# Kernel tuning notes

Hardware: AMD Instinct MI355X
Metric: run time of the kernel (lower is better)

The kernel has to match this reference:

```python
import jax, jax.numpy as jnp
import numpy as np

N_NODES = 100000
N_EDGES = 500000
D = 128          # node embedding dim; in_channels = 2*D = 256
HID = 256
OUT = 1


def setup_inputs() -> dict:
    key = jax.random.key(0)
    k1, k2, k3, k4, k5 = jax.random.split(key, 5)
    z = jax.random.normal(k1, (N_NODES, D), dtype=jnp.float32)
    z2 = jax.random.normal(k2, (N_NODES, D), dtype=jnp.float32)
    edge = jax.random.randint(k3, (2, N_EDGES), 0, N_NODES, dtype=jnp.int64)
    # MLP params (Linear stored as [in, out] for x @ W + b)
    W1 = jax.random.normal(k4, (2 * D, HID), dtype=jnp.float32) * (1.0 / np.sqrt(2 * D))
    b1 = jnp.zeros((HID,), dtype=jnp.float32)
    W2 = jax.random.normal(k5, (HID, OUT), dtype=jnp.float32) * (1.0 / np.sqrt(HID))
    b2 = jnp.zeros((OUT,), dtype=jnp.float32)
    return {"z": z, "z2": z2, "edge": edge, "W1": W1, "b1": b1, "W2": W2, "b2": b2}


def reference(z, z2, edge, W1, b1, W2, b2):
    # Gather node embeddings at edge endpoints, elementwise multiply, concat.
    src, dst = edge[0], edge[1]
    x = jnp.concatenate([z[src] * z[dst], z2[src] * z2[dst]], axis=1)  # [E, 2D]
    # Two-layer MLP (dropout is identity in eval mode), relu, final sigmoid.
    h = jax.nn.relu(x @ W1 + b1)        # [E, HID]
    out = jax.nn.sigmoid(h @ W2 + b2)   # [E, 1]
    return out
```

## Files before the change

kernel.cpp:

```cpp
#include <hip/hip_runtime.h>
#include <hip/hip_bf16.h>
#include <math.h>

typedef _Float16 half4 __attribute__((ext_vector_type(4)));
typedef _Float16 half8 __attribute__((ext_vector_type(8)));
typedef float f32x4 __attribute__((ext_vector_type(4)));

#define NE 500000
#define ND 128
#define NNODES 100000
#define NT ((NE + 63) / 64)
#define ZI_BLOCKS 12500

__global__ __launch_bounds__(256) void prep_all_kernel(
    const float* __restrict__ z, const float* __restrict__ z2,
    _Float16* __restrict__ zi,
    const float* __restrict__ W1, _Float16* __restrict__ w1p) {
    if (blockIdx.x < ZI_BLOCKS) {
        long t = (long)blockIdx.x * 256 + threadIdx.x;
        long idx = t * 8;
        int node = (int)(idx >> 8), col = (int)(idx & 255);
        const float* src = (col < 128) ? (z + (long)node * 128 + col)
                                       : (z2 + (long)node * 128 + (col - 128));
        float4 a = *reinterpret_cast<const float4*>(src);
        float4 b = *reinterpret_cast<const float4*>(src + 4);
        half8 v;
        v[0] = (_Float16)a.x; v[1] = (_Float16)a.y;
        v[2] = (_Float16)a.z; v[3] = (_Float16)a.w;
        v[4] = (_Float16)b.x; v[5] = (_Float16)b.y;
        v[6] = (_Float16)b.z; v[7] = (_Float16)b.w;
        *reinterpret_cast<half8*>(zi + idx) = v;
    } else {
        int i = (blockIdx.x - ZI_BLOCKS) * 256 + threadIdx.x;
        int j = i & 7;
        int lane = (i >> 3) & 63;
        int ks = (i >> 9) & 7;
        int nf = (i >> 12) & 3;
        int ni = i >> 14;
        int col = ni * 64 + nf * 16 + (lane & 15);
        int k = ks * 32 + (lane >> 4) * 8 + j;
        w1p[i] = (_Float16)W1[(long)k * 256 + col];
    }
}

template<int MIRROR>
__global__ __launch_bounds__(256, 4) void edge_mlp_v11(
    const float* __restrict__ z, const float* __restrict__ z2,
    const _Float16* __restrict__ zi,
    const int* __restrict__ edge,
    const _Float16* __restrict__ w1p,
    const float* __restrict__ b1, const float* __restrict__ W2,
    const float* __restrict__ b2, float* __restrict__ out)
{
    __shared__ _Float16 xs[64 * 256];
    __shared__ float ps[256];

    const int tid = threadIdx.x;
    const int lane = tid & 63;
    const int wv = tid >> 6;
    const int l15 = lane & 15;
    const int l4 = lane >> 4;
    const long eb0 = (long)blockIdx.x * 64;

    int idx;
    {
        long e = eb0 + wv * 16 + l15; if (e >= NE) e = NE - 1;
        idx = edge[(((lane >> 4) & 1) ? (long)NE : 0L) + e];
    }

    float b1v[4], w2v[4];
#pragma unroll
    for (int nf = 0; nf < 4; ++nf) {
        int col = wv * 64 + nf * 16 + l15;
        b1v[nf] = b1[col];
        w2v[nf] = W2[col];
    }
    const float bias2 = b2[0];

    if (MIRROR) {
        half4 vs[8], vd[8];
#pragma unroll
        for (int b = 0; b < 2; ++b) {
#pragma unroll
            for (int j = 0; j < 8; ++j) {
                int s = __builtin_amdgcn_readlane(idx, b * 8 + j);
                int d = __builtin_amdgcn_readlane(idx, 16 + b * 8 + j);
                vs[j] = *reinterpret_cast<const half4*>(zi + (long)s * 256 + lane * 4);
                vd[j] = *reinterpret_cast<const half4*>(zi + (long)d * 256 + lane * 4);
            }
#pragma unroll
            for (int j = 0; j < 8; ++j) {
                int e = wv * 16 + b * 8 + j;
                half4 p = vs[j] * vd[j];
                *reinterpret_cast<half4*>(
                    (char*)xs + e * 512 + ((lane * 8) ^ ((e & 7) << 4))) = p;
            }
        }
    } else {
        const float* zs = (lane < 32) ? z : z2;
        const int coff = (lane & 31) * 4;
#pragma unroll
        for (int b = 0; b < 4; ++b) {
            float4 fs[4], fd[4];
#pragma unroll
            for (int j = 0; j < 4; ++j) {
                int s = __builtin_amdgcn_readlane(idx, b * 4 + j);
                int d = __builtin_amdgcn_readlane(idx, 16 + b * 4 + j);
                fs[j] = *reinterpret_cast<const float4*>(zs + (long)s * ND + coff);
                fd[j] = *reinterpret_cast<const float4*>(zs + (long)d * ND + coff);
            }
#pragma unroll
            for (int j = 0; j < 4; ++j) {
                int e = wv * 16 + b * 4 + j;
                half4 p;
                p[0] = (_Float16)(fs[j].x * fd[j].x);
                p[1] = (_Float16)(fs[j].y * fd[j].y);
                p[2] = (_Float16)(fs[j].z * fd[j].z);
                p[3] = (_Float16)(fs[j].w * fd[j].w);
                *reinterpret_cast<half4*>(
                    (char*)xs + e * 512 + ((lane * 8) ^ ((e & 7) << 4))) = p;
            }
        }
    }
    __syncthreads();

    f32x4 acc[4][4];
#pragma unroll
    for (int mf = 0; mf < 4; ++mf)
#pragma unroll
        for (int nf = 0; nf < 4; ++nf)
            acc[mf][nf] = (f32x4){b1v[nf], b1v[nf], b1v[nf], b1v[nf]};

#pragma unroll
    for (int ks = 0; ks < 8; ++ks) {
        const int kb = ks * 64 + l4 * 16;
        half8 a[4], bfr[4];
#pragma unroll
        for (int mf = 0; mf < 4; ++mf) {
            int r = mf * 16 + l15;
            a[mf] = *reinterpret_cast<const half8*>(
                (const char*)xs + r * 512 + (kb ^ ((r & 7) << 4)));
        }
#pragma unroll
        for (int nf = 0; nf < 4; ++nf)
            bfr[nf] = *reinterpret_cast<const half8*>(
                w1p + (wv * 32 + nf * 8 + ks) * 512 + lane * 8);
#pragma unroll
        for (int mf = 0; mf < 4; ++mf)
#pragma unroll
            for (int nf = 0; nf < 4; ++nf)
                acc[mf][nf] = __builtin_amdgcn_mfma_f32_16x16x32_f16(
                    a[mf], bfr[nf], acc[mf][nf], 0, 0, 0);
    }

    float v[16];
#pragma unroll
    for (int mf = 0; mf < 4; ++mf)
#pragma unroll
        for (int r = 0; r < 4; ++r) {
            float s = 0.f;
#pragma unroll
            for (int nf = 0; nf < 4; ++nf)
                s += fmaxf(acc[mf][nf][r], 0.f) * w2v[nf];
            v[mf * 4 + r] = s;
        }
#pragma unroll
    for (int j = 0; j < 4; ++j) {
        const int m = 1 << j;
        const bool hi = (l15 & m) != 0;
#pragma unroll
        for (int p = 0; p < 16; p += 2 * m) {
            float snd = hi ? v[p] : v[p + m];
            float rcv = __shfl_xor(snd, m, 64);
            float kept = hi ? v[p + m] : v[p];
            v[p] = kept + rcv;
        }
    }
    {
        int row = (l15 >> 2) * 16 + l4 * 4 + (l15 & 3);
        ps[wv * 64 + row] = v[0];
    }
    __syncthreads();

    if (tid < 64) {
        float p = ps[tid] + ps[64 + tid] + ps[128 + tid] + ps[192 + tid] + bias2;
        long e = eb0 + tid;
        if (e < NE) out[e] = 1.0f / (1.0f + expf(-p));
    }
}

extern "C" void kernel_launch(void* const* d_in, const int* in_sizes, int n_in,
                              void* d_out, int out_size, void* d_ws, size_t ws_size,
                              hipStream_t stream)
{
    const float* z  = (const float*)d_in[0];
    const float* z2 = (const float*)d_in[1];
    const int*  edge = (const int*)d_in[2];
    const float* W1 = (const float*)d_in[3];
    const float* b1 = (const float*)d_in[4];
    const float* W2 = (const float*)d_in[5];
    const float* b2 = (const float*)d_in[6];
    float* out = (float*)d_out;

    const size_t zi_bytes = (size_t)NNODES * 256 * 2;
    const size_t w1_bytes = 256 * 256 * 2;
    const bool mirrors = (ws_size >= zi_bytes + w1_bytes);

    _Float16* zi  = (_Float16*)d_ws;
    _Float16* w1p = mirrors ? (_Float16*)((char*)d_ws + zi_bytes)
                            : (_Float16*)d_ws;

    if (mirrors) {
        prep_all_kernel<<<ZI_BLOCKS + 256, 256, 0, stream>>>(z, z2, zi, W1, w1p);
        edge_mlp_v11<1><<<NT, 256, 0, stream>>>(
            z, z2, zi, edge, w1p, b1, W2, b2, out);
    } else {
        prep_all_kernel<<<256, 256, 0, stream>>>(z, z2, (_Float16*)nullptr, W1, w1p);
        edge_mlp_v11<0><<<NT, 256, 0, stream>>>(
            z, z2, (const _Float16*)nullptr, edge, w1p, b1, W2, b2, out);
    }
}
```

Baseline: 132.3 us.

## Bucket-sort edges by source node before the fused edge MLP

Adds a histogram, a single-block scan and an atomic scatter pass that reorder edges into buckets keyed on source node index divided by 8. The main MLP kernel then reads the reordered source/destination indices and writes each result back to its original edge position. The aim is better cache locality for the source-side embedding gathers. In exchange it adds three extra kernel launches, atomic contention, extra index traffic and scattered output writes, while destination gathers stay random.

```diff
diff --git a/kernel.cpp b/kernel.cpp
--- a/kernel.cpp
+++ b/kernel.cpp
@@ -11,11 +11,20 @@
 #define NNODES 100000
 #define NT ((NE + 63) / 64)
 #define ZI_BLOCKS 12500
+#define W1_BLOCKS 256
+#define HIST_BLOCKS 977
+#define NB 12504
+
+__global__ __launch_bounds__(256) void zero_hist_kernel(int* __restrict__ hist) {
+    int i = blockIdx.x * 256 + threadIdx.x;
+    if (i < NB) hist[i] = 0;
+}
 
 __global__ __launch_bounds__(256) void prep_all_kernel(
     const float* __restrict__ z, const float* __restrict__ z2,
     _Float16* __restrict__ zi,
-    const float* __restrict__ W1, _Float16* __restrict__ w1p) {
+    const float* __restrict__ W1, _Float16* __restrict__ w1p,
+    const int* __restrict__ edge, int* __restrict__ hist, int do_hist) {
     if (blockIdx.x < ZI_BLOCKS) {
         long t = (long)blockIdx.x * 256 + threadIdx.x;
         long idx = t * 8;
@@ -30,7 +39,7 @@
         v[4] = (_Float16)b.x; v[5] = (_Float16)b.y;
         v[6] = (_Float16)b.z; v[7] = (_Float16)b.w;
         *reinterpret_cast<half8*>(zi + idx) = v;
-    } else {
+    } else if (blockIdx.x < ZI_BLOCKS + W1_BLOCKS) {
         int i = (blockIdx.x - ZI_BLOCKS) * 256 + threadIdx.x;
         int j = i & 7;
         int lane = (i >> 3) & 63;
@@ -40,14 +49,59 @@
         int col = ni * 64 + nf * 16 + (lane & 15);
         int k = ks * 32 + (lane >> 4) * 8 + j;
         w1p[i] = (_Float16)W1[(long)k * 256 + col];
-    }
-}
-
-template<int MIRROR>
-__global__ __launch_bounds__(256, 4) void edge_mlp_v11(
+    } else if (do_hist) {
+        int h = blockIdx.x - ZI_BLOCKS - W1_BLOCKS;
+        long e0 = (long)h * 512 + threadIdx.x;
+#pragma unroll
+        for (int r = 0; r < 2; ++r) {
+            long e = e0 + r * 256;
+            if (e < NE) atomicAdd(&hist[edge[e] >> 3], 1);
+        }
+    }
+}
+
+__global__ __launch_bounds__(256) void scan_kernel(
+    const int* __restrict__ hist, int* __restrict__ cursor) {
+    __shared__ int part[256];
+    const int t = threadIdx.x;
+    const int base = t * 49;
+    int s = 0;
+    for (int i = 0; i < 49; ++i) {
+        int idx = base + i;
+        if (idx < NB) s += hist[idx];
+    }
+    part[t] = s;
+    __syncthreads();
+    for (int off = 1; off < 256; off <<= 1) {
+        int v = (t >= off) ? part[t - off] : 0;
+        __syncthreads();
+        part[t] += v;
+        __syncthreads();
+    }
+    int run = (t == 0) ? 0 : part[t - 1];
+    for (int i = 0; i < 49; ++i) {
+        int idx = base + i;
+        if (idx < NB) { cursor[idx] = run; run += hist[idx]; }
+    }
+}
+
+__global__ __launch_bounds__(256) void scatter_kernel(
+    const int* __restrict__ edge, int* __restrict__ cursor,
+    int* __restrict__ ssrc, int* __restrict__ sdst, int* __restrict__ sorg) {
+    long e = (long)blockIdx.x * 256 + threadIdx.x;
+    if (e >= NE) return;
+    int s = edge[e], d = edge[NE + e];
+    int p = atomicAdd(&cursor[s >> 3], 1);
+    ssrc[p] = s; sdst[p] = d; sorg[p] = (int)e;
+}
+
+template<int MODE>
+__global__ __launch_bounds__(256, 4) void edge_mlp_v13(
     const float* __restrict__ z, const float* __restrict__ z2,
     const _Float16* __restrict__ zi,
     const int* __restrict__ edge,
+    const int* __restrict__ ssrc, const int* __restrict__ sdst,
+    const int* __restrict__ sorg,
     const _Float16* __restrict__ w1p,
     const float* __restrict__ b1, const float* __restrict__ W2,
     const float* __restrict__ b2, float* __restrict__ out)
@@ -65,7 +119,10 @@
     int idx;
     {
         long e = eb0 + wv * 16 + l15; if (e >= NE) e = NE - 1;
-        idx = edge[(((lane >> 4) & 1) ? (long)NE : 0L) + e];
+        if (MODE == 2)
+            idx = ((lane >> 4) & 1) ? sdst[e] : ssrc[e];
+        else
+            idx = edge[(((lane >> 4) & 1) ? (long)NE : 0L) + e];
     }
 
     float b1v[4], w2v[4];
@@ -77,7 +134,7 @@
     }
     const float bias2 = b2[0];
 
-    if (MIRROR) {
+    if (MODE >= 1) {
         half4 vs[8], vd[8];
 #pragma unroll
         for (int b = 0; b < 2; ++b) {
@@ -185,7 +242,11 @@
     if (tid < 64) {
         float p = ps[tid] + ps[64 + tid] + ps[128 + tid] + ps[192 + tid] + bias2;
         long e = eb0 + tid;
-        if (e < NE) out[e] = 1.0f / (1.0f + expf(-p));
+        if (e < NE) {
+            float r = 1.0f / (1.0f + expf(-p));
+            if (MODE == 2) out[sorg[e]] = r;
+            else           out[e] = r;
+        }
     }
 }
 
@@ -202,21 +263,42 @@
     const float* b2 = (const float*)d_in[6];
     float* out = (float*)d_out;
 
-    const size_t zi_bytes = (size_t)NNODES * 256 * 2;
-    const size_t w1_bytes = 256 * 256 * 2;
-    const bool mirrors = (ws_size >= zi_bytes + w1_bytes);
-
-    _Float16* zi  = (_Float16*)d_ws;
-    _Float16* w1p = mirrors ? (_Float16*)((char*)d_ws + zi_bytes)
-                            : (_Float16*)d_ws;
-
-    if (mirrors) {
-        prep_all_kernel<<<ZI_BLOCKS + 256, 256, 0, stream>>>(z, z2, zi, W1, w1p);
-        edge_mlp_v11<1><<<NT, 256, 0, stream>>>(
-            z, z2, zi, edge, w1p, b1, W2, b2, out);
+    const size_t zi_b   = (size_t)NNODES * 256 * 2;
+    const size_t w1_b   = 256 * 256 * 2;
+    const size_t sort_b = (size_t)NT * 64 * 4;
+    const size_t hist_b = (size_t)NB * 4;
+    const size_t need_mirror = zi_b + w1_b;
+    const size_t need_full   = need_mirror + 3 * sort_b + 2 * hist_b + 1024;
+
+    char* p = (char*)d_ws;
+    _Float16* zi  = (_Float16*)p;            p += zi_b;
+    _Float16* w1p = (_Float16*)p;            p += w1_b;
+    int* ssrc   = (int*)p;                   p += sort_b;
+    int* sdst   = (int*)p;                   p += sort_b;
+    int* sorg   = (int*)p;                   p += sort_b;
+    int* hist   = (int*)p;                   p += hist_b;
+    int* cursor = (int*)p;
+
+    if (ws_size >= need_full) {
+        zero_hist_kernel<<<(NB + 255) / 256, 256, 0, stream>>>(hist);
+        prep_all_kernel<<<ZI_BLOCKS + W1_BLOCKS + HIST_BLOCKS, 256, 0, stream>>>(
+            z, z2, zi, W1, w1p, edge, hist, 1);
+        scan_kernel<<<1, 256, 0, stream>>>(hist, cursor);
+        scatter_kernel<<<(NE + 255) / 256, 256, 0, stream>>>(
+            edge, cursor, ssrc, sdst, sorg);
+        edge_mlp_v13<2><<<NT, 256, 0, stream>>>(
+            z, z2, zi, edge, ssrc, sdst, sorg, w1p, b1, W2, b2, out);
+    } else if (ws_size >= need_mirror) {
+        _Float16* w1p2 = (_Float16*)((char*)d_ws + zi_b);
+        prep_all_kernel<<<ZI_BLOCKS + W1_BLOCKS, 256, 0, stream>>>(
+            z, z2, zi, W1, w1p2, edge, (int*)nullptr, 0);
+        edge_mlp_v13<1><<<NT, 256, 0, stream>>>(
+            z, z2, zi, edge, nullptr, nullptr, nullptr, w1p2, b1, W2, b2, out);
     } else {
-        prep_all_kernel<<<256, 256, 0, stream>>>(z, z2, (_Float16*)nullptr, W1, w1p);
-        edge_mlp_v11<0><<<NT, 256, 0, stream>>>(
-            z, z2, (const _Float16*)nullptr, edge, w1p, b1, W2, b2, out);
-    }
-}
+        _Float16* w1p2 = (_Float16*)d_ws;
+        prep_all_kernel<<<ZI_BLOCKS + W1_BLOCKS, 256, 0, stream>>>(
+            z, z2, (_Float16*)nullptr, W1, w1p2, edge, (int*)nullptr, 0);
+        edge_mlp_v13<0><<<NT, 256, 0, stream>>>(
+            z, z2, nullptr, edge, nullptr, nullptr, nullptr, w1p2, b1, W2, b2, out);
+    }
+}
```

New measurement: 207.9 us. 1.57x slower.
